# Kernel optimization log

Hardware: AMD Instinct MI355X
Metric: run time of the kernel (lower is better)

## Reference

```python
import jax, jax.numpy as jnp
import numpy as np

N_ROI, N_GRAPHS, HID, EDIM, EMB, NGRP = 116, 128, 64, 5, 16, 4
IN_CH, OUT_CH, N_LAYERS = 116, 2, 2


def _seg_softmax(scores, seg, num_segments):
    # numerically stable softmax over edges grouped by target node
    m = jax.ops.segment_max(scores, seg, num_segments=num_segments)
    ex = jnp.exp(scores - m[seg])
    s = jax.ops.segment_sum(ex, seg, num_segments=num_segments)
    return ex / (s[seg] + 1e-16)


def setup_inputs():
    key = jax.random.key(0)
    ks = jax.random.split(key, 16)
    N = N_ROI * N_GRAPHS
    idx = np.arange(N_ROI)
    s = np.repeat(idx, N_ROI)
    d = np.tile(idx, N_ROI)
    off = (np.arange(N_GRAPHS) * N_ROI)[:, None]
    src = (s[None, :] + off).reshape(-1)
    dst = (d[None, :] + off).reshape(-1)
    E = src.size

    def W(i, shp):
        fan = shp[-2] if len(shp) >= 2 else shp[-1]
        return jax.random.normal(ks[i], shp, jnp.float32) / np.sqrt(fan)

    def z(*shp):
        return jnp.zeros(shp, jnp.float32)

    return {
        "x": jax.random.normal(ks[0], (N, IN_CH), jnp.float32),
        "edge_attr": jax.random.normal(ks[1], (E, EDIM), jnp.float32),
        "emb": W(2, (NGRP, EMB)),
        "enc_W": W(3, (IN_CH + EMB, HID)), "enc_b": z(HID),
        "bn_g": jnp.ones((HID,), jnp.float32), "bn_b": z(HID),
        "gine_We": W(4, (EDIM, HID)), "gine_be": z(HID),
        "gine_W1": W(5, (HID, HID)), "gine_b1": z(HID),
        "gine_W2": W(6, (HID, HID)), "gine_b2": z(HID),
        "gat_Wl": W(7, (N_LAYERS, HID, HID)), "gat_bl": z(N_LAYERS, HID),
        "gat_Wr": W(8, (N_LAYERS, HID, HID)), "gat_br": z(N_LAYERS, HID),
        "gat_att": W(9, (N_LAYERS, HID)),
        "gat_We": W(10, (N_LAYERS, EDIM, HID)),
        "gat_bias": z(N_LAYERS, HID),
        "pool_W1": W(11, (HID, HID)), "pool_b1": z(HID), "pool_w2": W(12, (HID,)),
        "lin1_W": W(13, (HID, IN_CH)), "lin1_b": z(IN_CH),
        "lin2_W": W(14, (IN_CH, OUT_CH)), "lin2_b": z(OUT_CH),
        "edge_index": jnp.asarray(np.stack([src, dst]), jnp.int32),
        "batch": jnp.asarray(np.repeat(np.arange(N_GRAPHS), N_ROI), jnp.int32),
        "group_ids": jnp.asarray(np.tile(idx // 29, N_GRAPHS), jnp.int32),
        "num_graphs": N_GRAPHS,
    }


def reference(x, edge_attr, emb, enc_W, enc_b, bn_g, bn_b,
              gine_We, gine_be, gine_W1, gine_b1, gine_W2, gine_b2,
              gat_Wl, gat_bl, gat_Wr, gat_br, gat_att, gat_We, gat_bias,
              pool_W1, pool_b1, pool_w2, lin1_W, lin1_b, lin2_W, lin2_b,
              edge_index, batch, group_ids, num_graphs):
    src, dst = edge_index[0], edge_index[1]
    N = x.shape[0]
    # BrainEncodeEmbed: concat group embedding, linear, batchnorm (batch stats)
    h = jnp.concatenate([x, emb[group_ids]], axis=-1)          # [N, IN_CH+EMB]
    h = jax.nn.relu(h @ enc_W + enc_b)                          # [N, HID]
    mu = h.mean(0)
    var = h.var(0)
    h = (h - mu) * jax.lax.rsqrt(var + 1e-5) * bn_g + bn_b
    # GINEConv (eps=0): sum_j relu(x_j + lin_edge(e_ij)), then MLP
    e = edge_attr @ gine_We + gine_be                           # [E, HID]
    agg = jax.ops.segment_sum(jax.nn.relu(h[src] + e), dst, num_segments=N)
    h = h + agg
    h = jax.nn.relu(h @ gine_W1 + gine_b1) @ gine_W2 + gine_b2
    h = jax.nn.relu(h)
    # GATv2 layers (heads=1, concat=False)
    for l in range(N_LAYERS):
        xl = h @ gat_Wl[l] + gat_bl[l]                          # [N, HID]
        xr = h @ gat_Wr[l] + gat_br[l]
        zed = jax.nn.leaky_relu(xl[src] + xr[dst] + edge_attr @ gat_We[l], 0.2)
        alpha = _seg_softmax(zed @ gat_att[l], dst, N)          # [E]
        h = jax.nn.relu(
            jax.ops.segment_sum(xl[src] * alpha[:, None], dst, num_segments=N)
            + gat_bias[l])
    # AttentionPooling: global softmax over all nodes, scatter-add by graph
    w = jax.nn.softmax(jnp.tanh(h @ pool_W1 + pool_b1) @ pool_w2, axis=0)
    pooled = jax.ops.segment_sum(h * w[:, None], batch, num_segments=num_graphs)
    return jax.nn.relu(pooled @ lin1_W + lin1_b) @ lin2_W + lin2_b
```

## Files before the change

### kernel.cpp

```cpp
#include <hip/hip_runtime.h>
#include <math.h>

#define R    116
#define R2   (116*116)
#define G    128
#define NN   (R*G)
#define HID  64
#define EDIM 5
#define INCH 116
#define EMBD 16

__device__ __forceinline__ float waveReduceSum(float v) {
#pragma unroll
    for (int m = 32; m >= 1; m >>= 1) v += __shfl_xor(v, m, 64);
    return v;
}

__global__ __launch_bounds__(256) void k_etr(
    const float* __restrict__ ea, float* __restrict__ eat) {
    int b = blockIdx.x;
    int g = b >> 4;
    int t = b & 15;
    int i0 = (t >> 2) << 5, j0 = (t & 3) << 5;
    int ni = min(32, R - i0), nj = min(32, R - j0);
    __shared__ float tile[32][165];
    const float* src = ea + ((size_t)(g*R + i0)*R + j0)*EDIM;
    int tot = ni * nj * EDIM;
    for (int idx = threadIdx.x; idx < tot; idx += 256) {
        int ii = idx / (nj*EDIM);
        int rem = idx - ii*(nj*EDIM);
        tile[ii][rem] = src[(size_t)ii*R*EDIM + rem];
    }
    __syncthreads();
    float* dst = eat + ((size_t)(g*R + j0)*R + i0)*EDIM;
    int tot2 = nj * ni * EDIM;
    for (int idx = threadIdx.x; idx < tot2; idx += 256) {
        int jj = idx / (ni*EDIM);
        int rem = idx - jj*(ni*EDIM);
        int ii = rem / EDIM, e = rem - ii*EDIM;
        dst[(size_t)jj*R*EDIM + rem] = tile[ii][jj*EDIM + e];
    }
}

__global__ __launch_bounds__(256) void k_encode(
    const float* __restrict__ x, const float* __restrict__ emb,
    const int* __restrict__ group_ids,
    const float* __restrict__ W, const float* __restrict__ bvec,
    float* __restrict__ h) {
    int w = threadIdx.x >> 6, lane = threadIdx.x & 63;
    int n = blockIdx.x*4 + w;
    __shared__ float xin[4][136];
    for (int idx = lane; idx < INCH; idx += 64) xin[w][idx] = x[(size_t)n*INCH + idx];
    if (lane < EMBD) xin[w][INCH + lane] = emb[group_ids[n]*EMBD + lane];
    float acc = bvec[lane];
#pragma unroll
    for (int k = 0; k < INCH + EMBD; k += 4) {
        float4 q = *(const float4*)&xin[w][k];
        acc = fmaf(q.x, W[(k  )*HID + lane], acc);
        acc = fmaf(q.y, W[(k+1)*HID + lane], acc);
        acc = fmaf(q.z, W[(k+2)*HID + lane], acc);
        acc = fmaf(q.w, W[(k+3)*HID + lane], acc);
    }
    h[(size_t)n*HID + lane] = fmaxf(acc, 0.f);
}

__global__ __launch_bounds__(256) void k_stats_partial(
    const float* __restrict__ h, float* __restrict__ partials) {
    int b = blockIdx.x;
    int tid = threadIdx.x;
    int c = tid & 63, r0 = tid >> 6;
    float s = 0.f, s2 = 0.f;
    int row0 = b*64;
#pragma unroll
    for (int k = 0; k < 16; ++k) {
        float v = h[(size_t)(row0 + r0 + 4*k)*HID + c];
        s += v; s2 += v*v;
    }
    __shared__ float ls[256], l2[256];
    ls[tid] = s; l2[tid] = s2;
    __syncthreads();
    if (tid < 64) {
        s  = ls[tid] + ls[tid+64] + ls[tid+128] + ls[tid+192];
        s2 = l2[tid] + l2[tid+64] + l2[tid+128] + l2[tid+192];
        partials[b*128 + tid]      = s;
        partials[b*128 + 64 + tid] = s2;
    }
}

__global__ __launch_bounds__(64) void k_stats_final(
    const float* __restrict__ partials, const float* __restrict__ gam,
    const float* __restrict__ bet, float* __restrict__ stats) {
    int c = threadIdx.x;
    float s = 0.f, s2 = 0.f;
    for (int b = 0; b < NN/64; ++b) {
        s  += partials[b*128 + c];
        s2 += partials[b*128 + 64 + c];
    }
    float mu  = s / (float)NN;
    float var = s2 / (float)NN - mu*mu;
    float rs  = rsqrtf(var + 1e-5f);
    float sc  = rs * gam[c];
    stats[c]      = sc;
    stats[64 + c] = bet[c] - mu*sc;
}

__global__ __launch_bounds__(256) void k_gine(
    const float* __restrict__ h, const float* __restrict__ stats,
    const float* __restrict__ eat,
    const float* __restrict__ We, const float* __restrict__ be,
    const float* __restrict__ W1, const float* __restrict__ b1,
    const float* __restrict__ W2, const float* __restrict__ b2,
    float* __restrict__ hout) {
    int b = blockIdx.x;
    int g = b & (G-1), chunk = b >> 7;
    int j0 = chunk*20, jcnt = min(20, R - j0);
    int tid = threadIdx.x, w = tid >> 6, lane = tid & 63;
    __shared__ float hs[R][64];
    __shared__ float eac[4][R*8];
    __shared__ float t1s[4][68];
    size_t hbase = (size_t)g*R*HID;
    float scv = stats[lane], shv = stats[64 + lane];
    for (int idx = tid; idx < R*HID; idx += 256)
        hs[idx>>6][lane] = fmaf(h[hbase + idx], scv, shv);
    float w0=We[lane], w1v=We[64+lane], w2v=We[128+lane],
          w3v=We[192+lane], w4v=We[256+lane], bec=be[lane];
    __syncthreads();
    for (int jj = w; jj < jcnt; jj += 4) {
        int j = j0 + jj;
        const float* colp = eat + (size_t)(g*R + j)*R*EDIM;
        for (int idx = lane; idx < R*EDIM; idx += 64) {
            int i = idx / EDIM, e = idx - i*EDIM;
            eac[w][i*8 + e] = colp[idx];
        }
        float agg = 0.f;
        for (int i = 0; i < R; ++i) {
            float4 q = *(const float4*)&eac[w][i*8];
            float q4 = eac[w][i*8 + 4];
            float ew = bec;
            ew = fmaf(q.x, w0, ew); ew = fmaf(q.y, w1v, ew);
            ew = fmaf(q.z, w2v, ew); ew = fmaf(q.w, w3v, ew);
            ew = fmaf(q4, w4v, ew);
            agg += fmaxf(hs[i][lane] + ew, 0.f);
        }
        float h1 = hs[j][lane] + agg;
        t1s[w][lane] = h1;
        float acc = b1[lane];
#pragma unroll
        for (int k = 0; k < HID; k += 4) {
            float4 tq = *(const float4*)&t1s[w][k];
            acc = fmaf(tq.x, W1[(k  )*HID + lane], acc);
            acc = fmaf(tq.y, W1[(k+1)*HID + lane], acc);
            acc = fmaf(tq.z, W1[(k+2)*HID + lane], acc);
            acc = fmaf(tq.w, W1[(k+3)*HID + lane], acc);
        }
        float t2 = fmaxf(acc, 0.f);
        t1s[w][lane] = t2;
        float acc2 = b2[lane];
#pragma unroll
        for (int k = 0; k < HID; k += 4) {
            float4 tq = *(const float4*)&t1s[w][k];
            acc2 = fmaf(tq.x, W2[(k  )*HID + lane], acc2);
            acc2 = fmaf(tq.y, W2[(k+1)*HID + lane], acc2);
            acc2 = fmaf(tq.z, W2[(k+2)*HID + lane], acc2);
            acc2 = fmaf(tq.w, W2[(k+3)*HID + lane], acc2);
        }
        hout[hbase + (size_t)j*HID + lane] = fmaxf(acc2, 0.f);
    }
}

__global__ __launch_bounds__(256) void k_xlxr(
    const float* __restrict__ h,
    const float* __restrict__ Wl, const float* __restrict__ bl,
    const float* __restrict__ Wr, const float* __restrict__ br,
    const float* __restrict__ att,
    float* __restrict__ xl, float* __restrict__ xr,
    float* __restrict__ axl, float* __restrict__ axr) {
    int w = threadIdx.x >> 6, lane = threadIdx.x & 63;
    int n = blockIdx.x*4 + w;
    __shared__ float hr[4][68];
    hr[w][lane] = h[(size_t)n*HID + lane];
    float aL = bl[lane], aR = br[lane];
#pragma unroll
    for (int k = 0; k < HID; k += 4) {
        float4 q = *(const float4*)&hr[w][k];
        aL = fmaf(q.x, Wl[(k  )*HID + lane], aL);
        aR = fmaf(q.x, Wr[(k  )*HID + lane], aR);
        aL = fmaf(q.y, Wl[(k+1)*HID + lane], aL);
        aR = fmaf(q.y, Wr[(k+1)*HID + lane], aR);
        aL = fmaf(q.z, Wl[(k+2)*HID + lane], aL);
        aR = fmaf(q.z, Wr[(k+2)*HID + lane], aR);
        aL = fmaf(q.w, Wl[(k+3)*HID + lane], aL);
        aR = fmaf(q.w, Wr[(k+3)*HID + lane], aR);
    }
    xl[(size_t)n*HID + lane] = aL;
    xr[(size_t)n*HID + lane] = aR;
    float at = att[lane];
    float pL = waveReduceSum(aL * at);
    float pR = waveReduceSum(aR * at);
    if (lane == 0) { axl[n] = pL; axr[n] = pR; }
}

__global__ __launch_bounds__(256) void k_gat(
    const float* __restrict__ xl, const float* __restrict__ xr,
    const float* __restrict__ axlg, const float* __restrict__ axrg,
    const float* __restrict__ eat, const float* __restrict__ We,
    const float* __restrict__ att, const float* __restrict__ bias,
    float* __restrict__ hout) {
    int b = blockIdx.x;
    int g = b & (G-1), chunk = b >> 7;
    int j0 = chunk*15, jcnt = min(15, R - j0);
    int tid = threadIdx.x, w = tid >> 6, lane = tid & 63;
    __shared__ float xls[R][65];
    __shared__ float we_s[64][8];
    __shared__ float xrs[15][64];
    __shared__ float axl_s[R];
    __shared__ float axr_s[16];
    __shared__ float ps[4][120];
    __shared__ float bias_s[64];
    __shared__ float was[8];
    size_t hbase = (size_t)g*R*HID;
    for (int idx = tid; idx < R*HID; idx += 256)
        xls[idx>>6][idx&63] = xl[hbase + idx];
    for (int idx = tid; idx < jcnt*HID; idx += 256)
        xrs[idx>>6][idx&63] = xr[hbase + (size_t)j0*HID + idx];
    if (tid < R) axl_s[tid] = axlg[g*R + tid];
    else if (tid < R + 16) {
        int q = tid - R;
        axr_s[q] = (q < jcnt) ? axrg[g*R + j0 + q] : 0.f;
    }
    if (tid >= 192) bias_s[tid - 192] = bias[tid - 192];
    if (w == 1) {
        float g0=We[lane], g1=We[64+lane], g2=We[128+lane],
              g3=We[192+lane], g4=We[256+lane], at=att[lane];
        we_s[lane][0]=g0; we_s[lane][1]=g1; we_s[lane][2]=g2; we_s[lane][3]=g3;
        we_s[lane][4]=g4; we_s[lane][5]=at; we_s[lane][6]=0.f; we_s[lane][7]=0.f;
        float p0 = waveReduceSum(g0*at);
        float p1 = waveReduceSum(g1*at);
        float p2 = waveReduceSum(g2*at);
        float p3 = waveReduceSum(g3*at);
        float p4 = waveReduceSum(g4*at);
        if (lane == 0) { was[0]=p0; was[1]=p1; was[2]=p2; was[3]=p3; was[4]=p4; }
    }
    __syncthreads();

    bool vB = lane < (R - 64);
    int rb = vB ? (64 + lane) : lane;
    for (int jj = w; jj < jcnt; jj += 4) {
        int j = j0 + jj;
        const float* colp = eat + (size_t)(g*R + j)*R*EDIM;
        const float* ca = colp + (size_t)lane*EDIM;
        float a0=ca[0], a1=ca[1], a2=ca[2], a3=ca[3], a4=ca[4];
        float b0=0.f, b1v=0.f, b2v=0.f, b3v=0.f, b4v=0.f;
        if (vB) {
            const float* cb = colp + (size_t)rb*EDIM;
            b0=cb[0]; b1v=cb[1]; b2v=cb[2]; b3v=cb[3]; b4v=cb[4];
        }
        float base = axr_s[jj];
        float LA = axl_s[lane] + base;
        LA = fmaf(a0,was[0],LA); LA = fmaf(a1,was[1],LA); LA = fmaf(a2,was[2],LA);
        LA = fmaf(a3,was[3],LA); LA = fmaf(a4,was[4],LA);
        float LB = axl_s[rb] + base;
        LB = fmaf(b0,was[0],LB); LB = fmaf(b1v,was[1],LB); LB = fmaf(b2v,was[2],LB);
        LB = fmaf(b3v,was[3],LB); LB = fmaf(b4v,was[4],LB);
        float accA = 0.f, accB = 0.f;
#pragma unroll 4
        for (int c = 0; c < HID; ++c) {
            float4 qa = *(const float4*)&we_s[c][0];
            float2 qb = *(const float2*)&we_s[c][4];
            float u  = xrs[jj][c];
            float zA = xls[lane][c] + u;
            zA = fmaf(a0,qa.x,zA); zA = fmaf(a1,qa.y,zA); zA = fmaf(a2,qa.z,zA);
            zA = fmaf(a3,qa.w,zA); zA = fmaf(a4,qb.x,zA);
            float zB = xls[rb][c] + u;
            zB = fmaf(b0,qa.x,zB); zB = fmaf(b1v,qa.y,zB); zB = fmaf(b2v,qa.z,zB);
            zB = fmaf(b3v,qa.w,zB); zB = fmaf(b4v,qb.x,zB);
            accA = fmaf(__builtin_fabsf(zA), qb.y, accA);
            accB = fmaf(__builtin_fabsf(zB), qb.y, accB);
        }
        float sA = fmaf(0.4f, accA, 0.6f*LA);
        float sB = vB ? fmaf(0.4f, accB, 0.6f*LB) : -1e30f;
        float m = fmaxf(sA, sB);
#pragma unroll
        for (int msk = 32; msk >= 1; msk >>= 1) m = fmaxf(m, __shfl_xor(m, msk, 64));
        float eA = __expf(sA - m);
        float eB = vB ? __expf(sB - m) : 0.f;
        float s = eA + eB;
#pragma unroll
        for (int msk = 32; msk >= 1; msk >>= 1) s += __shfl_xor(s, msk, 64);
        float inv = 1.f / (s + 1e-16f);
        ps[w][lane] = eA * inv;
        if (vB) ps[w][64 + lane] = eB * inv;
        float o = 0.f;
#pragma unroll 4
        for (int i = 0; i < R; i += 4) {
            float4 p4 = *(const float4*)&ps[w][i];
            o = fmaf(p4.x, xls[i  ][lane], o);
            o = fmaf(p4.y, xls[i+1][lane], o);
            o = fmaf(p4.z, xls[i+2][lane], o);
            o = fmaf(p4.w, xls[i+3][lane], o);
        }
        hout[hbase + (size_t)j*HID + lane] = fmaxf(o + bias_s[lane], 0.f);
    }
}

__global__ __launch_bounds__(256) void k_pool_score(
    const float* __restrict__ h, const float* __restrict__ W1,
    const float* __restrict__ b1, const float* __restrict__ w2,
    float* __restrict__ scores) {
    int w = threadIdx.x >> 6, lane = threadIdx.x & 63;
    int n = blockIdx.x*4 + w;
    __shared__ float hr[4][68];
    hr[w][lane] = h[(size_t)n*HID + lane];
    float acc = b1[lane];
#pragma unroll
    for (int k = 0; k < HID; k += 4) {
        float4 q = *(const float4*)&hr[w][k];
        acc = fmaf(q.x, W1[(k  )*HID + lane], acc);
        acc = fmaf(q.y, W1[(k+1)*HID + lane], acc);
        acc = fmaf(q.z, W1[(k+2)*HID + lane], acc);
        acc = fmaf(q.w, W1[(k+3)*HID + lane], acc);
    }
    float p = tanhf(acc) * w2[lane];
    p = waveReduceSum(p);
    if (lane == 0) scores[n] = p;
}

__global__ __launch_bounds__(1024) void k_pool_reduce(
    const float* __restrict__ scores, float* __restrict__ ms) {
    __shared__ float red[1024];
    int tid = threadIdx.x;
    float m = -1e30f;
    for (int i = tid; i < NN; i += 1024) m = fmaxf(m, scores[i]);
    red[tid] = m;
    __syncthreads();
    for (int s = 512; s > 0; s >>= 1) {
        if (tid < s) red[tid] = fmaxf(red[tid], red[tid+s]);
        __syncthreads();
    }
    float mx = red[0];
    __syncthreads();
    float sum = 0.f;
    for (int i = tid; i < NN; i += 1024) sum += __expf(scores[i] - mx);
    red[tid] = sum;
    __syncthreads();
    for (int s = 512; s > 0; s >>= 1) {
        if (tid < s) red[tid] += red[tid+s];
        __syncthreads();
    }
    if (tid == 0) { ms[0] = mx; ms[1] = red[0]; }
}

__global__ __launch_bounds__(64) void k_pool_final(
    const float* __restrict__ h, const float* __restrict__ scores,
    const float* __restrict__ ms,
    const float* __restrict__ lin1W, const float* __restrict__ lin1b,
    const float* __restrict__ lin2W, const float* __restrict__ lin2b,
    float* __restrict__ out) {
    int g = blockIdx.x, c = threadIdx.x;
    float mx = ms[0], inv = 1.f / ms[1];
    float pc = 0.f;
    int nb = g*R;
    for (int r = 0; r < R; ++r) {
        float wv = __expf(scores[nb + r] - mx) * inv;
        pc = fmaf(h[(size_t)(nb + r)*HID + c], wv, pc);
    }
    __shared__ float pl[HID];
    __shared__ float t[INCH];
    pl[c] = pc;
    __syncthreads();
    for (int k = c; k < INCH; k += 64) {
        float acc = lin1b[k];
#pragma unroll 8
        for (int q = 0; q < HID; ++q) acc = fmaf(pl[q], lin1W[q*INCH + k], acc);
        t[k] = fmaxf(acc, 0.f);
    }
    __syncthreads();
    if (c < 2) {
        float o = lin2b[c];
        for (int k = 0; k < INCH; ++k) o = fmaf(t[k], lin2W[k*2 + c], o);
        out[g*2 + c] = o;
    }
}

extern "C" void kernel_launch(void* const* d_in, const int* in_sizes, int n_in,
                              void* d_out, int out_size, void* d_ws, size_t ws_size,
                              hipStream_t stream) {
    (void)in_sizes; (void)n_in; (void)out_size; (void)ws_size;
    const float* x        = (const float*)d_in[0];
    const float* edge_attr= (const float*)d_in[1];
    const float* emb      = (const float*)d_in[2];
    const float* enc_W    = (const float*)d_in[3];
    const float* enc_b    = (const float*)d_in[4];
    const float* bn_g     = (const float*)d_in[5];
    const float* bn_b     = (const float*)d_in[6];
    const float* gine_We  = (const float*)d_in[7];
    const float* gine_be  = (const float*)d_in[8];
    const float* gine_W1  = (const float*)d_in[9];
    const float* gine_b1  = (const float*)d_in[10];
    const float* gine_W2  = (const float*)d_in[11];
    const float* gine_b2  = (const float*)d_in[12];
    const float* gat_Wl   = (const float*)d_in[13];
    const float* gat_bl   = (const float*)d_in[14];
    const float* gat_Wr   = (const float*)d_in[15];
    const float* gat_br   = (const float*)d_in[16];
    const float* gat_att  = (const float*)d_in[17];
    const float* gat_We   = (const float*)d_in[18];
    const float* gat_bias = (const float*)d_in[19];
    const float* pool_W1  = (const float*)d_in[20];
    const float* pool_b1  = (const float*)d_in[21];
    const float* pool_w2  = (const float*)d_in[22];
    const float* lin1_W   = (const float*)d_in[23];
    const float* lin1_b   = (const float*)d_in[24];
    const float* lin2_W   = (const float*)d_in[25];
    const float* lin2_b   = (const float*)d_in[26];
    const int*   group_ids= (const int*)d_in[29];
    float* out = (float*)d_out;

    float* w = (float*)d_ws;
    float* eat      = w;
    float* hA       = eat + (size_t)R2*G*EDIM;
    float* hB       = hA + (size_t)NN*HID;
    float* xlb      = hB + (size_t)NN*HID;
    float* xrb      = xlb + (size_t)NN*HID;
    float* axl      = xrb + (size_t)NN*HID;
    float* axr      = axl + NN;
    float* scores   = axr + NN;
    float* partials = scores + NN;
    float* stats    = partials + (NN/64)*128;
    float* pms      = stats + 128;

    k_etr<<<G*16, 256, 0, stream>>>(edge_attr, eat);
    k_encode<<<NN/4, 256, 0, stream>>>(x, emb, group_ids, enc_W, enc_b, hA);
    k_stats_partial<<<NN/64, 256, 0, stream>>>(hA, partials);
    k_stats_final<<<1, 64, 0, stream>>>(partials, bn_g, bn_b, stats);
    k_gine<<<G*6, 256, 0, stream>>>(hA, stats, eat, gine_We, gine_be,
                                    gine_W1, gine_b1, gine_W2, gine_b2, hB);
    k_xlxr<<<NN/4, 256, 0, stream>>>(hB, gat_Wl, gat_bl, gat_Wr, gat_br,
                                     gat_att, xlb, xrb, axl, axr);
    k_gat<<<G*8, 256, 0, stream>>>(xlb, xrb, axl, axr, eat, gat_We,
                                   gat_att, gat_bias, hA);
    k_xlxr<<<NN/4, 256, 0, stream>>>(hA, gat_Wl + HID*HID, gat_bl + HID,
                                     gat_Wr + HID*HID, gat_br + HID,
                                     gat_att + HID, xlb, xrb, axl, axr);
    k_gat<<<G*8, 256, 0, stream>>>(xlb, xrb, axl, axr, eat, gat_We + EDIM*HID,
                                   gat_att + HID, gat_bias + HID, hB);
    k_pool_score<<<NN/4, 256, 0, stream>>>(hB, pool_W1, pool_b1, pool_w2, scores);
    k_pool_reduce<<<1, 1024, 0, stream>>>(scores, pms);
    k_pool_final<<<G, 64, 0, stream>>>(hB, scores, pms, lin1_W, lin1_b,
                                       lin2_W, lin2_b, out);
}
```

Baseline: 266.2 us.

## Process four target nodes per wave jointly in GINE and GATv2 kernels

```diff
diff --git a/kernel.cpp b/kernel.cpp
--- a/kernel.cpp
+++ b/kernel.cpp
@@ -104,7 +104,7 @@
     stats[64 + c] = bet[c] - mu*sc;
 }
 
-__global__ __launch_bounds__(256) void k_gine(
+__global__ __launch_bounds__(256, 4) void k_gine(
     const float* __restrict__ h, const float* __restrict__ stats,
     const float* __restrict__ eat,
     const float* __restrict__ We, const float* __restrict__ be,
@@ -113,10 +113,9 @@
     float* __restrict__ hout) {
     int b = blockIdx.x;
     int g = b & (G-1), chunk = b >> 7;
-    int j0 = chunk*20, jcnt = min(20, R - j0);
+    int j0 = chunk*15;
     int tid = threadIdx.x, w = tid >> 6, lane = tid & 63;
     __shared__ float hs[R][64];
-    __shared__ float eac[4][R*8];
     __shared__ float t1s[4][68];
     size_t hbase = (size_t)g*R*HID;
     float scv = stats[lane], shv = stats[64 + lane];
@@ -125,24 +124,44 @@
     float w0=We[lane], w1v=We[64+lane], w2v=We[128+lane],
           w3v=We[192+lane], w4v=We[256+lane], bec=be[lane];
     __syncthreads();
-    for (int jj = w; jj < jcnt; jj += 4) {
+
+    bool act[4]; int jv[4];
+    const float* cp[4];
+#pragma unroll
+    for (int t = 0; t < 4; ++t) {
+        int jj = w + 4*t;
         int j = j0 + jj;
-        const float* colp = eat + (size_t)(g*R + j)*R*EDIM;
-        for (int idx = lane; idx < R*EDIM; idx += 64) {
-            int i = idx / EDIM, e = idx - i*EDIM;
-            eac[w][i*8 + e] = colp[idx];
-        }
-        float agg = 0.f;
-        for (int i = 0; i < R; ++i) {
-            float4 q = *(const float4*)&eac[w][i*8];
-            float q4 = eac[w][i*8 + 4];
-            float ew = bec;
-            ew = fmaf(q.x, w0, ew); ew = fmaf(q.y, w1v, ew);
-            ew = fmaf(q.z, w2v, ew); ew = fmaf(q.w, w3v, ew);
-            ew = fmaf(q4, w4v, ew);
-            agg += fmaxf(hs[i][lane] + ew, 0.f);
-        }
-        float h1 = hs[j][lane] + agg;
+        act[t] = (jj < 15) && (j < R);
+        jv[t] = act[t] ? j : (R-1);
+        cp[t] = eat + (size_t)(g*R + jv[t])*R*EDIM;
+    }
+    float agg0 = 0.f, agg1 = 0.f, agg2 = 0.f, agg3 = 0.f;
+    for (int i = 0; i < R; ++i) {
+        float hv = hs[i][lane];
+        float4 q0, q1, q2, q3;
+        __builtin_memcpy(&q0, cp[0] + i*EDIM, 16); float q04 = cp[0][i*EDIM+4];
+        __builtin_memcpy(&q1, cp[1] + i*EDIM, 16); float q14 = cp[1][i*EDIM+4];
+        __builtin_memcpy(&q2, cp[2] + i*EDIM, 16); float q24 = cp[2][i*EDIM+4];
+        __builtin_memcpy(&q3, cp[3] + i*EDIM, 16); float q34 = cp[3][i*EDIM+4];
+        float e0 = bec, e1 = bec, e2 = bec, e3 = bec;
+        e0 = fmaf(q0.x,w0,e0); e0 = fmaf(q0.y,w1v,e0); e0 = fmaf(q0.z,w2v,e0);
+        e0 = fmaf(q0.w,w3v,e0); e0 = fmaf(q04,w4v,e0);
+        e1 = fmaf(q1.x,w0,e1); e1 = fmaf(q1.y,w1v,e1); e1 = fmaf(q1.z,w2v,e1);
+        e1 = fmaf(q1.w,w3v,e1); e1 = fmaf(q14,w4v,e1);
+        e2 = fmaf(q2.x,w0,e2); e2 = fmaf(q2.y,w1v,e2); e2 = fmaf(q2.z,w2v,e2);
+        e2 = fmaf(q2.w,w3v,e2); e2 = fmaf(q24,w4v,e2);
+        e3 = fmaf(q3.x,w0,e3); e3 = fmaf(q3.y,w1v,e3); e3 = fmaf(q3.z,w2v,e3);
+        e3 = fmaf(q3.w,w3v,e3); e3 = fmaf(q34,w4v,e3);
+        agg0 += fmaxf(hv + e0, 0.f);
+        agg1 += fmaxf(hv + e1, 0.f);
+        agg2 += fmaxf(hv + e2, 0.f);
+        agg3 += fmaxf(hv + e3, 0.f);
+    }
+    float aggs[4] = {agg0, agg1, agg2, agg3};
+#pragma unroll
+    for (int t = 0; t < 4; ++t) {
+        if (!act[t]) continue;
+        float h1 = hs[jv[t]][lane] + aggs[t];
         t1s[w][lane] = h1;
         float acc = b1[lane];
 #pragma unroll
@@ -153,8 +172,7 @@
             acc = fmaf(tq.z, W1[(k+2)*HID + lane], acc);
             acc = fmaf(tq.w, W1[(k+3)*HID + lane], acc);
         }
-        float t2 = fmaxf(acc, 0.f);
-        t1s[w][lane] = t2;
+        t1s[w][lane] = fmaxf(acc, 0.f);
         float acc2 = b2[lane];
 #pragma unroll
         for (int k = 0; k < HID; k += 4) {
@@ -164,7 +182,7 @@
             acc2 = fmaf(tq.z, W2[(k+2)*HID + lane], acc2);
             acc2 = fmaf(tq.w, W2[(k+3)*HID + lane], acc2);
         }
-        hout[hbase + (size_t)j*HID + lane] = fmaxf(acc2, 0.f);
+        hout[hbase + (size_t)jv[t]*HID + lane] = fmaxf(acc2, 0.f);
     }
 }
 
@@ -200,7 +218,7 @@
     if (lane == 0) { axl[n] = pL; axr[n] = pR; }
 }
 
-__global__ __launch_bounds__(256) void k_gat(
+__global__ __launch_bounds__(256, 4) void k_gat(
     const float* __restrict__ xl, const float* __restrict__ xr,
     const float* __restrict__ axlg, const float* __restrict__ axrg,
     const float* __restrict__ eat, const float* __restrict__ We,
@@ -208,99 +226,119 @@
     float* __restrict__ hout) {
     int b = blockIdx.x;
     int g = b & (G-1), chunk = b >> 7;
-    int j0 = chunk*15, jcnt = min(15, R - j0);
+    int j0 = chunk*15;
     int tid = threadIdx.x, w = tid >> 6, lane = tid & 63;
     __shared__ float xls[R][65];
     __shared__ float we_s[64][8];
-    __shared__ float xrs[15][64];
-    __shared__ float axl_s[R];
-    __shared__ float axr_s[16];
-    __shared__ float ps[4][120];
-    __shared__ float bias_s[64];
-    __shared__ float was[8];
+    __shared__ float ps[4][2][120];
+    __shared__ float was_s[8];
     size_t hbase = (size_t)g*R*HID;
     for (int idx = tid; idx < R*HID; idx += 256)
         xls[idx>>6][idx&63] = xl[hbase + idx];
-    for (int idx = tid; idx < jcnt*HID; idx += 256)
-        xrs[idx>>6][idx&63] = xr[hbase + (size_t)j0*HID + idx];
-    if (tid < R) axl_s[tid] = axlg[g*R + tid];
-    else if (tid < R + 16) {
-        int q = tid - R;
-        axr_s[q] = (q < jcnt) ? axrg[g*R + j0 + q] : 0.f;
-    }
-    if (tid >= 192) bias_s[tid - 192] = bias[tid - 192];
     if (w == 1) {
         float g0=We[lane], g1=We[64+lane], g2=We[128+lane],
               g3=We[192+lane], g4=We[256+lane], at=att[lane];
-        we_s[lane][0]=g0; we_s[lane][1]=g1; we_s[lane][2]=g2; we_s[lane][3]=g3;
-        we_s[lane][4]=g4; we_s[lane][5]=at; we_s[lane][6]=0.f; we_s[lane][7]=0.f;
+        we_s[lane][0]=g0; we_s[lane][1]=g1; we_s[lane][2]=g2;
+        we_s[lane][3]=g3; we_s[lane][4]=g4; we_s[lane][5]=at;
+        we_s[lane][6]=0.f; we_s[lane][7]=0.f;
         float p0 = waveReduceSum(g0*at);
         float p1 = waveReduceSum(g1*at);
         float p2 = waveReduceSum(g2*at);
         float p3 = waveReduceSum(g3*at);
         float p4 = waveReduceSum(g4*at);
-        if (lane == 0) { was[0]=p0; was[1]=p1; was[2]=p2; was[3]=p3; was[4]=p4; }
-    }
-    __syncthreads();
-
+        if (lane == 0) { was_s[0]=p0; was_s[1]=p1; was_s[2]=p2;
+                         was_s[3]=p3; was_s[4]=p4; }
+    }
+    __syncthreads();
+    float wasv0=was_s[0], wasv1=was_s[1], wasv2=was_s[2],
+          wasv3=was_s[3], wasv4=was_s[4];
+    float biasv = bias[lane];
     bool vB = lane < (R - 64);
     int rb = vB ? (64 + lane) : lane;
-    for (int jj = w; jj < jcnt; jj += 4) {
+    float axA = axlg[g*R + lane];
+    float axB = axlg[g*R + rb];
+
+    bool act[4]; int jv[4];
+    float axr_[4];
+    float eA[4][5], eB[4][5];
+#pragma unroll
+    for (int t = 0; t < 4; ++t) {
+        int jj = w + 4*t;
         int j = j0 + jj;
-        const float* colp = eat + (size_t)(g*R + j)*R*EDIM;
-        const float* ca = colp + (size_t)lane*EDIM;
-        float a0=ca[0], a1=ca[1], a2=ca[2], a3=ca[3], a4=ca[4];
-        float b0=0.f, b1v=0.f, b2v=0.f, b3v=0.f, b4v=0.f;
-        if (vB) {
-            const float* cb = colp + (size_t)rb*EDIM;
-            b0=cb[0]; b1v=cb[1]; b2v=cb[2]; b3v=cb[3]; b4v=cb[4];
+        act[t] = (jj < 15) && (j < R);
+        jv[t] = act[t] ? j : (R-1);
+        axr_[t] = axrg[g*R + jv[t]];
+        const float* cp = eat + (size_t)(g*R + jv[t])*R*EDIM;
+#pragma unroll
+        for (int e = 0; e < 5; ++e) eA[t][e] = cp[lane*EDIM + e];
+#pragma unroll
+        for (int e = 0; e < 5; ++e) eB[t][e] = cp[rb*EDIM + e];
+    }
+    const float* xrg = xr + hbase;
+    float accA[4] = {0,0,0,0}, accB[4] = {0,0,0,0};
+#pragma unroll 4
+    for (int c = 0; c < HID; ++c) {
+        float4 qa = *(const float4*)&we_s[c][0];
+        float2 qb = *(const float2*)&we_s[c][4];
+        float xA = xls[lane][c];
+        float xB = xls[rb][c];
+#pragma unroll
+        for (int t = 0; t < 4; ++t) {
+            float u = xrg[(size_t)jv[t]*HID + c];
+            float zA = xA + u;
+            zA = fmaf(eA[t][0],qa.x,zA); zA = fmaf(eA[t][1],qa.y,zA);
+            zA = fmaf(eA[t][2],qa.z,zA); zA = fmaf(eA[t][3],qa.w,zA);
+            zA = fmaf(eA[t][4],qb.x,zA);
+            accA[t] = fmaf(__builtin_fabsf(zA), qb.y, accA[t]);
+            float zB = xB + u;
+            zB = fmaf(eB[t][0],qa.x,zB); zB = fmaf(eB[t][1],qa.y,zB);
+            zB = fmaf(eB[t][2],qa.z,zB); zB = fmaf(eB[t][3],qa.w,zB);
+            zB = fmaf(eB[t][4],qb.x,zB);
+            accB[t] = fmaf(__builtin_fabsf(zB), qb.y, accB[t]);
         }
-        float base = axr_s[jj];
-        float LA = axl_s[lane] + base;
-        LA = fmaf(a0,was[0],LA); LA = fmaf(a1,was[1],LA); LA = fmaf(a2,was[2],LA);
-        LA = fmaf(a3,was[3],LA); LA = fmaf(a4,was[4],LA);
-        float LB = axl_s[rb] + base;
-        LB = fmaf(b0,was[0],LB); LB = fmaf(b1v,was[1],LB); LB = fmaf(b2v,was[2],LB);
-        LB = fmaf(b3v,was[3],LB); LB = fmaf(b4v,was[4],LB);
-        float accA = 0.f, accB = 0.f;
-#pragma unroll 4
-        for (int c = 0; c < HID; ++c) {
-            float4 qa = *(const float4*)&we_s[c][0];
-            float2 qb = *(const float2*)&we_s[c][4];
-            float u  = xrs[jj][c];
-            float zA = xls[lane][c] + u;
-            zA = fmaf(a0,qa.x,zA); zA = fmaf(a1,qa.y,zA); zA = fmaf(a2,qa.z,zA);
-            zA = fmaf(a3,qa.w,zA); zA = fmaf(a4,qb.x,zA);
-            float zB = xls[rb][c] + u;
-            zB = fmaf(b0,qa.x,zB); zB = fmaf(b1v,qa.y,zB); zB = fmaf(b2v,qa.z,zB);
-            zB = fmaf(b3v,qa.w,zB); zB = fmaf(b4v,qb.x,zB);
-            accA = fmaf(__builtin_fabsf(zA), qb.y, accA);
-            accB = fmaf(__builtin_fabsf(zB), qb.y, accB);
-        }
-        float sA = fmaf(0.4f, accA, 0.6f*LA);
-        float sB = vB ? fmaf(0.4f, accB, 0.6f*LB) : -1e30f;
+    }
+    float o[4];
+#pragma unroll
+    for (int t = 0; t < 4; ++t) {
+        float LA = axA + axr_[t], LB = axB + axr_[t];
+        LA = fmaf(eA[t][0],wasv0,LA); LA = fmaf(eA[t][1],wasv1,LA);
+        LA = fmaf(eA[t][2],wasv2,LA); LA = fmaf(eA[t][3],wasv3,LA);
+        LA = fmaf(eA[t][4],wasv4,LA);
+        LB = fmaf(eB[t][0],wasv0,LB); LB = fmaf(eB[t][1],wasv1,LB);
+        LB = fmaf(eB[t][2],wasv2,LB); LB = fmaf(eB[t][3],wasv3,LB);
+        LB = fmaf(eB[t][4],wasv4,LB);
+        float sA = fmaf(0.4f, accA[t], 0.6f*LA);
+        float sB = vB ? fmaf(0.4f, accB[t], 0.6f*LB) : -1e30f;
         float m = fmaxf(sA, sB);
 #pragma unroll
         for (int msk = 32; msk >= 1; msk >>= 1) m = fmaxf(m, __shfl_xor(m, msk, 64));
-        float eA = __expf(sA - m);
-        float eB = vB ? __expf(sB - m) : 0.f;
-        float s = eA + eB;
+        float eAx = __expf(sA - m);
+        float eBx = vB ? __expf(sB - m) : 0.f;
+        float s = eAx + eBx;
 #pragma unroll
         for (int msk = 32; msk >= 1; msk >>= 1) s += __shfl_xor(s, msk, 64);
         float inv = 1.f / (s + 1e-16f);
-        ps[w][lane] = eA * inv;
-        if (vB) ps[w][64 + lane] = eB * inv;
-        float o = 0.f;
-#pragma unroll 4
-        for (int i = 0; i < R; i += 4) {
-            float4 p4 = *(const float4*)&ps[w][i];
-            o = fmaf(p4.x, xls[i  ][lane], o);
-            o = fmaf(p4.y, xls[i+1][lane], o);
-            o = fmaf(p4.z, xls[i+2][lane], o);
-            o = fmaf(p4.w, xls[i+3][lane], o);
+        ps[w][t&1][lane] = eAx * inv;
+        if (vB) ps[w][t&1][64 + lane] = eBx * inv;
+        if (t & 1) {
+            float o0 = 0.f, o1 = 0.f;
+            for (int i = 0; i < R; i += 4) {
+                float4 p0 = *(const float4*)&ps[w][0][i];
+                float4 p1 = *(const float4*)&ps[w][1][i];
+                float x0 = xls[i  ][lane], x1 = xls[i+1][lane];
+                float x2 = xls[i+2][lane], x3 = xls[i+3][lane];
+                o0 = fmaf(p0.x,x0,o0); o0 = fmaf(p0.y,x1,o0);
+                o0 = fmaf(p0.z,x2,o0); o0 = fmaf(p0.w,x3,o0);
+                o1 = fmaf(p1.x,x0,o1); o1 = fmaf(p1.y,x1,o1);
+                o1 = fmaf(p1.z,x2,o1); o1 = fmaf(p1.w,x3,o1);
+            }
+            o[t-1] = o0; o[t] = o1;
         }
-        hout[hbase + (size_t)j*HID + lane] = fmaxf(o + bias_s[lane], 0.f);
-    }
+    }
+#pragma unroll
+    for (int t = 0; t < 4; ++t)
+        if (act[t])
+            hout[hbase + (size_t)jv[t]*HID + lane] = fmaxf(o[t] + biasv, 0.f);
 }
 
 __global__ __launch_bounds__(256) void k_pool_score(
@@ -433,7 +471,7 @@
     k_encode<<<NN/4, 256, 0, stream>>>(x, emb, group_ids, enc_W, enc_b, hA);
     k_stats_partial<<<NN/64, 256, 0, stream>>>(hA, partials);
     k_stats_final<<<1, 64, 0, stream>>>(partials, bn_g, bn_b, stats);
-    k_gine<<<G*6, 256, 0, stream>>>(hA, stats, eat, gine_We, gine_be,
+    k_gine<<<G*8, 256, 0, stream>>>(hA, stats, eat, gine_We, gine_be,
                                     gine_W1, gine_b1, gine_W2, gine_b2, hB);
     k_xlxr<<<NN/4, 256, 0, stream>>>(hB, gat_Wl, gat_bl, gat_Wr, gat_br,
                                      gat_att, xlb, xrb, axl, axr);
```

New measurement: 918.8 us. +245.1%, slower.

## Register-block GINE over 8 targets and hoist GAT weight prep out of blocks

Applied to the files above, without the earlier changes.

```diff
diff --git a/kernel.cpp b/kernel.cpp
--- a/kernel.cpp
+++ b/kernel.cpp
@@ -42,6 +42,28 @@
     }
 }
 
+__global__ __launch_bounds__(64) void k_prep(
+    const float* __restrict__ We, const float* __restrict__ att,
+    float* __restrict__ wepack, float* __restrict__ was2) {
+    int l = blockIdx.x, c = threadIdx.x;
+    const float* Wl = We + l*EDIM*HID;
+    const float* al = att + l*HID;
+    float g0=Wl[c], g1=Wl[64+c], g2=Wl[128+c], g3=Wl[192+c], g4=Wl[256+c];
+    float at = al[c];
+    float* wp = wepack + l*HID*8 + c*8;
+    wp[0]=g0; wp[1]=g1; wp[2]=g2; wp[3]=g3; wp[4]=g4; wp[5]=at;
+    wp[6]=0.f; wp[7]=0.f;
+    float p0 = waveReduceSum(g0*at);
+    float p1 = waveReduceSum(g1*at);
+    float p2 = waveReduceSum(g2*at);
+    float p3 = waveReduceSum(g3*at);
+    float p4 = waveReduceSum(g4*at);
+    if (c == 0) {
+        float* ws = was2 + l*8;
+        ws[0]=p0; ws[1]=p1; ws[2]=p2; ws[3]=p3; ws[4]=p4;
+    }
+}
+
 __global__ __launch_bounds__(256) void k_encode(
     const float* __restrict__ x, const float* __restrict__ emb,
     const int* __restrict__ group_ids,
@@ -106,17 +128,16 @@
 
 __global__ __launch_bounds__(256) void k_gine(
     const float* __restrict__ h, const float* __restrict__ stats,
-    const float* __restrict__ eat,
+    const float* __restrict__ ea,
     const float* __restrict__ We, const float* __restrict__ be,
     const float* __restrict__ W1, const float* __restrict__ b1,
     const float* __restrict__ W2, const float* __restrict__ b2,
     float* __restrict__ hout) {
     int b = blockIdx.x;
-    int g = b & (G-1), chunk = b >> 7;
-    int j0 = chunk*20, jcnt = min(20, R - j0);
+    int g = b & (G-1), q = b >> 7;
     int tid = threadIdx.x, w = tid >> 6, lane = tid & 63;
+    int j0 = min(q*32 + w*8, R - 8);
     __shared__ float hs[R][64];
-    __shared__ float eac[4][R*8];
     __shared__ float t1s[4][68];
     size_t hbase = (size_t)g*R*HID;
     float scv = stats[lane], shv = stats[64 + lane];
@@ -125,46 +146,48 @@
     float w0=We[lane], w1v=We[64+lane], w2v=We[128+lane],
           w3v=We[192+lane], w4v=We[256+lane], bec=be[lane];
     __syncthreads();
-    for (int jj = w; jj < jcnt; jj += 4) {
-        int j = j0 + jj;
-        const float* colp = eat + (size_t)(g*R + j)*R*EDIM;
-        for (int idx = lane; idx < R*EDIM; idx += 64) {
-            int i = idx / EDIM, e = idx - i*EDIM;
-            eac[w][i*8 + e] = colp[idx];
-        }
-        float agg = 0.f;
-        for (int i = 0; i < R; ++i) {
-            float4 q = *(const float4*)&eac[w][i*8];
-            float q4 = eac[w][i*8 + 4];
+
+    float acc[8] = {0.f,0.f,0.f,0.f,0.f,0.f,0.f,0.f};
+    int sbase = __builtin_amdgcn_readfirstlane((g*R*R + j0)*EDIM);
+    for (int i = 0; i < R; ++i) {
+        float hv = hs[i][lane];
+        const float* sp = ea + sbase + i*(R*EDIM);
+#pragma unroll
+        for (int j = 0; j < 8; ++j) {
             float ew = bec;
-            ew = fmaf(q.x, w0, ew); ew = fmaf(q.y, w1v, ew);
-            ew = fmaf(q.z, w2v, ew); ew = fmaf(q.w, w3v, ew);
-            ew = fmaf(q4, w4v, ew);
-            agg += fmaxf(hs[i][lane] + ew, 0.f);
-        }
-        float h1 = hs[j][lane] + agg;
+            ew = fmaf(sp[j*5+0], w0,  ew);
+            ew = fmaf(sp[j*5+1], w1v, ew);
+            ew = fmaf(sp[j*5+2], w2v, ew);
+            ew = fmaf(sp[j*5+3], w3v, ew);
+            ew = fmaf(sp[j*5+4], w4v, ew);
+            acc[j] += fmaxf(hv + ew, 0.f);
+        }
+    }
+#pragma unroll
+    for (int j = 0; j < 8; ++j) {
+        int jd = j0 + j;
+        float h1 = hs[jd][lane] + acc[j];
         t1s[w][lane] = h1;
-        float acc = b1[lane];
+        float a1 = b1[lane];
 #pragma unroll
         for (int k = 0; k < HID; k += 4) {
             float4 tq = *(const float4*)&t1s[w][k];
-            acc = fmaf(tq.x, W1[(k  )*HID + lane], acc);
-            acc = fmaf(tq.y, W1[(k+1)*HID + lane], acc);
-            acc = fmaf(tq.z, W1[(k+2)*HID + lane], acc);
-            acc = fmaf(tq.w, W1[(k+3)*HID + lane], acc);
-        }
-        float t2 = fmaxf(acc, 0.f);
-        t1s[w][lane] = t2;
-        float acc2 = b2[lane];
+            a1 = fmaf(tq.x, W1[(k  )*HID + lane], a1);
+            a1 = fmaf(tq.y, W1[(k+1)*HID + lane], a1);
+            a1 = fmaf(tq.z, W1[(k+2)*HID + lane], a1);
+            a1 = fmaf(tq.w, W1[(k+3)*HID + lane], a1);
+        }
+        t1s[w][lane] = fmaxf(a1, 0.f);
+        float a2 = b2[lane];
 #pragma unroll
         for (int k = 0; k < HID; k += 4) {
             float4 tq = *(const float4*)&t1s[w][k];
-            acc2 = fmaf(tq.x, W2[(k  )*HID + lane], acc2);
-            acc2 = fmaf(tq.y, W2[(k+1)*HID + lane], acc2);
-            acc2 = fmaf(tq.z, W2[(k+2)*HID + lane], acc2);
-            acc2 = fmaf(tq.w, W2[(k+3)*HID + lane], acc2);
-        }
-        hout[hbase + (size_t)j*HID + lane] = fmaxf(acc2, 0.f);
+            a2 = fmaf(tq.x, W2[(k  )*HID + lane], a2);
+            a2 = fmaf(tq.y, W2[(k+1)*HID + lane], a2);
+            a2 = fmaf(tq.z, W2[(k+2)*HID + lane], a2);
+            a2 = fmaf(tq.w, W2[(k+3)*HID + lane], a2);
+        }
+        hout[hbase + (size_t)jd*HID + lane] = fmaxf(a2, 0.f);
     }
 }
 
@@ -203,93 +226,92 @@
 __global__ __launch_bounds__(256) void k_gat(
     const float* __restrict__ xl, const float* __restrict__ xr,
     const float* __restrict__ axlg, const float* __restrict__ axrg,
-    const float* __restrict__ eat, const float* __restrict__ We,
-    const float* __restrict__ att, const float* __restrict__ bias,
+    const float* __restrict__ eat, const float* __restrict__ wepack,
+    const float* __restrict__ wasg, const float* __restrict__ bias,
     float* __restrict__ hout) {
     int b = blockIdx.x;
     int g = b & (G-1), chunk = b >> 7;
     int j0 = chunk*15, jcnt = min(15, R - j0);
     int tid = threadIdx.x, w = tid >> 6, lane = tid & 63;
-    __shared__ float xls[R][65];
-    __shared__ float we_s[64][8];
-    __shared__ float xrs[15][64];
-    __shared__ float axl_s[R];
-    __shared__ float axr_s[16];
+    __shared__ float xls[R][66];
     __shared__ float ps[4][120];
-    __shared__ float bias_s[64];
-    __shared__ float was[8];
     size_t hbase = (size_t)g*R*HID;
     for (int idx = tid; idx < R*HID; idx += 256)
         xls[idx>>6][idx&63] = xl[hbase + idx];
-    for (int idx = tid; idx < jcnt*HID; idx += 256)
-        xrs[idx>>6][idx&63] = xr[hbase + (size_t)j0*HID + idx];
-    if (tid < R) axl_s[tid] = axlg[g*R + tid];
-    else if (tid < R + 16) {
-        int q = tid - R;
-        axr_s[q] = (q < jcnt) ? axrg[g*R + j0 + q] : 0.f;
-    }
-    if (tid >= 192) bias_s[tid - 192] = bias[tid - 192];
-    if (w == 1) {
-        float g0=We[lane], g1=We[64+lane], g2=We[128+lane],
-              g3=We[192+lane], g4=We[256+lane], at=att[lane];
-        we_s[lane][0]=g0; we_s[lane][1]=g1; we_s[lane][2]=g2; we_s[lane][3]=g3;
-        we_s[lane][4]=g4; we_s[lane][5]=at; we_s[lane][6]=0.f; we_s[lane][7]=0.f;
-        float p0 = waveReduceSum(g0*at);
-        float p1 = waveReduceSum(g1*at);
-        float p2 = waveReduceSum(g2*at);
-        float p3 = waveReduceSum(g3*at);
-        float p4 = waveReduceSum(g4*at);
-        if (lane == 0) { was[0]=p0; was[1]=p1; was[2]=p2; was[3]=p3; was[4]=p4; }
-    }
-    __syncthreads();
-
+    float biasv = bias[lane];
+    float wasv0 = wasg[0], wasv1 = wasg[1], wasv2 = wasg[2],
+          wasv3 = wasg[3], wasv4 = wasg[4];
     bool vB = lane < (R - 64);
     int rb = vB ? (64 + lane) : lane;
+    float axA = axlg[g*R + lane];
+    float axB = axlg[g*R + rb];
+    __syncthreads();
+
     for (int jj = w; jj < jcnt; jj += 4) {
         int j = j0 + jj;
         const float* colp = eat + (size_t)(g*R + j)*R*EDIM;
-        const float* ca = colp + (size_t)lane*EDIM;
-        float a0=ca[0], a1=ca[1], a2=ca[2], a3=ca[3], a4=ca[4];
-        float b0=0.f, b1v=0.f, b2v=0.f, b3v=0.f, b4v=0.f;
-        if (vB) {
-            const float* cb = colp + (size_t)rb*EDIM;
-            b0=cb[0]; b1v=cb[1]; b2v=cb[2]; b3v=cb[3]; b4v=cb[4];
-        }
-        float base = axr_s[jj];
-        float LA = axl_s[lane] + base;
-        LA = fmaf(a0,was[0],LA); LA = fmaf(a1,was[1],LA); LA = fmaf(a2,was[2],LA);
-        LA = fmaf(a3,was[3],LA); LA = fmaf(a4,was[4],LA);
-        float LB = axl_s[rb] + base;
-        LB = fmaf(b0,was[0],LB); LB = fmaf(b1v,was[1],LB); LB = fmaf(b2v,was[2],LB);
-        LB = fmaf(b3v,was[3],LB); LB = fmaf(b4v,was[4],LB);
+        float eA[5], eB[5];
+#pragma unroll
+        for (int e = 0; e < 5; ++e) {
+            eA[e] = colp[lane*EDIM + e];
+            eB[e] = colp[rb*EDIM + e];
+        }
+        const float* xrp = xr + hbase + (size_t)j*HID;
+        float axrj = axrg[g*R + j];
         float accA = 0.f, accB = 0.f;
 #pragma unroll 4
-        for (int c = 0; c < HID; ++c) {
-            float4 qa = *(const float4*)&we_s[c][0];
-            float2 qb = *(const float2*)&we_s[c][4];
-            float u  = xrs[jj][c];
-            float zA = xls[lane][c] + u;
-            zA = fmaf(a0,qa.x,zA); zA = fmaf(a1,qa.y,zA); zA = fmaf(a2,qa.z,zA);
-            zA = fmaf(a3,qa.w,zA); zA = fmaf(a4,qb.x,zA);
-            float zB = xls[rb][c] + u;
-            zB = fmaf(b0,qa.x,zB); zB = fmaf(b1v,qa.y,zB); zB = fmaf(b2v,qa.z,zB);
-            zB = fmaf(b3v,qa.w,zB); zB = fmaf(b4v,qb.x,zB);
-            accA = fmaf(__builtin_fabsf(zA), qb.y, accA);
-            accB = fmaf(__builtin_fabsf(zB), qb.y, accB);
-        }
+        for (int c = 0; c < HID; c += 2) {
+            float2 xA2 = *(const float2*)&xls[lane][c];
+            float2 xB2 = *(const float2*)&xls[rb][c];
+            {
+                const float* wp = wepack + c*8;
+                float u = xrp[c];
+                float zA = xA2.x + u;
+                zA = fmaf(eA[0],wp[0],zA); zA = fmaf(eA[1],wp[1],zA);
+                zA = fmaf(eA[2],wp[2],zA); zA = fmaf(eA[3],wp[3],zA);
+                zA = fmaf(eA[4],wp[4],zA);
+                accA = fmaf(__builtin_fabsf(zA), wp[5], accA);
+                float zB = xB2.x + u;
+                zB = fmaf(eB[0],wp[0],zB); zB = fmaf(eB[1],wp[1],zB);
+                zB = fmaf(eB[2],wp[2],zB); zB = fmaf(eB[3],wp[3],zB);
+                zB = fmaf(eB[4],wp[4],zB);
+                accB = fmaf(__builtin_fabsf(zB), wp[5], accB);
+            }
+            {
+                const float* wp = wepack + (c+1)*8;
+                float u = xrp[c+1];
+                float zA = xA2.y + u;
+                zA = fmaf(eA[0],wp[0],zA); zA = fmaf(eA[1],wp[1],zA);
+                zA = fmaf(eA[2],wp[2],zA); zA = fmaf(eA[3],wp[3],zA);
+                zA = fmaf(eA[4],wp[4],zA);
+                accA = fmaf(__builtin_fabsf(zA), wp[5], accA);
+                float zB = xB2.y + u;
+                zB = fmaf(eB[0],wp[0],zB); zB = fmaf(eB[1],wp[1],zB);
+                zB = fmaf(eB[2],wp[2],zB); zB = fmaf(eB[3],wp[3],zB);
+                zB = fmaf(eB[4],wp[4],zB);
+                accB = fmaf(__builtin_fabsf(zB), wp[5], accB);
+            }
+        }
+        float LA = axA + axrj, LB = axB + axrj;
+        LA = fmaf(eA[0],wasv0,LA); LA = fmaf(eA[1],wasv1,LA);
+        LA = fmaf(eA[2],wasv2,LA); LA = fmaf(eA[3],wasv3,LA);
+        LA = fmaf(eA[4],wasv4,LA);
+        LB = fmaf(eB[0],wasv0,LB); LB = fmaf(eB[1],wasv1,LB);
+        LB = fmaf(eB[2],wasv2,LB); LB = fmaf(eB[3],wasv3,LB);
+        LB = fmaf(eB[4],wasv4,LB);
         float sA = fmaf(0.4f, accA, 0.6f*LA);
         float sB = vB ? fmaf(0.4f, accB, 0.6f*LB) : -1e30f;
         float m = fmaxf(sA, sB);
 #pragma unroll
         for (int msk = 32; msk >= 1; msk >>= 1) m = fmaxf(m, __shfl_xor(m, msk, 64));
-        float eA = __expf(sA - m);
-        float eB = vB ? __expf(sB - m) : 0.f;
-        float s = eA + eB;
+        float eAx = __expf(sA - m);
+        float eBx = vB ? __expf(sB - m) : 0.f;
+        float s = eAx + eBx;
 #pragma unroll
         for (int msk = 32; msk >= 1; msk >>= 1) s += __shfl_xor(s, msk, 64);
         float inv = 1.f / (s + 1e-16f);
-        ps[w][lane] = eA * inv;
-        if (vB) ps[w][64 + lane] = eB * inv;
+        ps[w][lane] = eAx * inv;
+        if (vB) ps[w][64 + lane] = eBx * inv;
         float o = 0.f;
 #pragma unroll 4
         for (int i = 0; i < R; i += 4) {
@@ -299,7 +321,7 @@
             o = fmaf(p4.z, xls[i+2][lane], o);
             o = fmaf(p4.w, xls[i+3][lane], o);
         }
-        hout[hbase + (size_t)j*HID + lane] = fmaxf(o + bias_s[lane], 0.f);
+        hout[hbase + (size_t)j*HID + lane] = fmaxf(o + biasv, 0.f);
     }
 }
 
@@ -428,22 +450,25 @@
     float* partials = scores + NN;
     float* stats    = partials + (NN/64)*128;
     float* pms      = stats + 128;
+    float* wepack   = pms + 2;
+    float* was2     = wepack + 2*HID*8;
 
     k_etr<<<G*16, 256, 0, stream>>>(edge_attr, eat);
+    k_prep<<<2, 64, 0, stream>>>(gat_We, gat_att, wepack, was2);
     k_encode<<<NN/4, 256, 0, stream>>>(x, emb, group_ids, enc_W, enc_b, hA);
     k_stats_partial<<<NN/64, 256, 0, stream>>>(hA, partials);
     k_stats_final<<<1, 64, 0, stream>>>(partials, bn_g, bn_b, stats);
-    k_gine<<<G*6, 256, 0, stream>>>(hA, stats, eat, gine_We, gine_be,
+    k_gine<<<G*4, 256, 0, stream>>>(hA, stats, edge_attr, gine_We, gine_be,
                                     gine_W1, gine_b1, gine_W2, gine_b2, hB);
     k_xlxr<<<NN/4, 256, 0, stream>>>(hB, gat_Wl, gat_bl, gat_Wr, gat_br,
                                      gat_att, xlb, xrb, axl, axr);
-    k_gat<<<G*8, 256, 0, stream>>>(xlb, xrb, axl, axr, eat, gat_We,
-                                   gat_att, gat_bias, hA);
+    k_gat<<<G*8, 256, 0, stream>>>(xlb, xrb, axl, axr, eat, wepack,
+                                   was2, gat_bias, hA);
     k_xlxr<<<NN/4, 256, 0, stream>>>(hA, gat_Wl + HID*HID, gat_bl + HID,
                                      gat_Wr + HID*HID, gat_br + HID,
                                      gat_att + HID, xlb, xrb, axl, axr);
-    k_gat<<<G*8, 256, 0, stream>>>(xlb, xrb, axl, axr, eat, gat_We + EDIM*HID,
-                                   gat_att + HID, gat_bias + HID, hB);
+    k_gat<<<G*8, 256, 0, stream>>>(xlb, xrb, axl, axr, eat, wepack + HID*8,
+                                   was2 + 8, gat_bias + HID, hB);
     k_pool_score<<<NN/4, 256, 0, stream>>>(hB, pool_W1, pool_b1, pool_w2, scores);
     k_pool_reduce<<<1, 1024, 0, stream>>>(scores, pms);
     k_pool_final<<<G, 64, 0, stream>>>(hB, scores, pms, lin1_W, lin1_b,
```

Result: no change. 267.9 us (median of 2 runs) (+0.6%).
